# Kernel optimization log

Measured on AMD Instinct MI355X. Metric: run time of the kernel, lower is better.

The kernel has to match this reference:

```python
import jax, jax.numpy as jnp
import numpy as np

S, B, F, U = 8, 65536, 256, 256  # N_species, N_batch, N_feats, N_units (depth=2)


def setup_inputs() -> dict:
    key = jax.random.key(0)
    ks = jax.random.split(key, 9)
    b = jax.random.normal(ks[0], (S, B, F), dtype=jnp.float32)
    # Per-species weights stacked along species axis (equivalent to ModuleList of Linears).
    # nn.Linear default init: U(-1/sqrt(fan_in), 1/sqrt(fan_in)) -- exact dist doesn't matter
    # for a correctness baseline; scale similarly.
    def lin(k, fan_in, shape):
        lim = 1.0 / np.sqrt(fan_in)
        return jax.random.uniform(k, shape, dtype=jnp.float32, minval=-lim, maxval=lim)
    W1 = lin(ks[1], F, (S, F, U)); b1 = lin(ks[2], F, (S, U))
    W2 = lin(ks[3], U, (S, U, U)); b2 = lin(ks[4], U, (S, U))
    W3 = lin(ks[5], U, (S, U, U)); b3 = lin(ks[6], U, (S, U))
    W4 = lin(ks[7], U, (S, U, 1)); b4 = lin(ks[8], U, (S, 1))
    return {"b": b, "W1": W1, "b1": b1, "W2": W2, "b2": b2,
            "W3": W3, "b3": b3, "W4": W4, "b4": b4}


def _leaky(x):
    return jnp.where(x >= 0, x, 0.1 * x)  # LeakyReLU(0.1)


def reference(b, W1, b1, W2, b2, W3, b3, W4, b4):
    # depth == 2 path. Dropout(p=0.01) is identity in eval mode.
    # Per-species batched GEMMs: (S,B,in) x (S,in,out) -> (S,B,out)
    x = _leaky(jnp.einsum('sbf,sfu->sbu', b, W1) + b1[:, None, :])
    x = _leaky(jnp.einsum('sbu,suv->sbv', x, W2) + b2[:, None, :])
    x = _leaky(jnp.einsum('sbu,suv->sbv', x, W3) + b3[:, None, :])
    A = jnp.einsum('sbu,suo->sbo', x, W4) + b4[:, None, :]  # (S, B, 1)
    return jax.nn.sigmoid(A.sum(axis=0))  # (B, 1)
```

## Files before the change

kernel.cpp:

```cpp
#include <hip/hip_runtime.h>

typedef __bf16 bf16x8 __attribute__((ext_vector_type(8)));
typedef float  f32x4  __attribute__((ext_vector_type(4)));
typedef float  fvec4  __attribute__((ext_vector_type(4)));

#define NSPEC 8
#define NB    65536
#define NF    256

__global__ __launch_bounds__(256) void wconv_kernel(
    const float* __restrict__ W1, const float* __restrict__ W2,
    const float* __restrict__ W3, __bf16* __restrict__ WT)
{
    __shared__ float tile[32][33];
    int bid = blockIdx.x;
    int l   = bid >> 9;
    int rem = bid & 511;
    int s   = rem >> 6;
    int tt  = rem & 63;
    int ti  = tt >> 3, tj = tt & 7;
    const float* W   = (l == 0) ? W1 : (l == 1) ? W2 : W3;
    const float* ibs = W + (size_t)s * 65536;
    int c  = threadIdx.x & 31;
    int r0 = threadIdx.x >> 5;
#pragma unroll
    for (int k = 0; k < 4; ++k) {
        int r = r0 + k * 8;
        tile[r][c] = ibs[(ti * 32 + r) * 256 + tj * 32 + c];
    }
    __syncthreads();
    __bf16* obs = WT + ((size_t)(l * 8 + s)) * 65536;
#pragma unroll
    for (int k = 0; k < 4; ++k) {
        int r = r0 + k * 8;
        obs[(tj * 32 + r) * 256 + ti * 32 + c] = (__bf16)tile[c][r];
    }
}

#define GLLD(gp, lp)                                                     \
    __builtin_amdgcn_global_load_lds(                                    \
        (const __attribute__((address_space(1))) char*)(gp),             \
        (__attribute__((address_space(3))) char*)(lp), 16, 0, 0)

#define BAR()                                                            \
    do {                                                                 \
        __builtin_amdgcn_sched_barrier(0);                               \
        asm volatile("s_waitcnt lgkmcnt(0)" ::: "memory");               \
        __builtin_amdgcn_s_barrier();                                    \
        __builtin_amdgcn_sched_barrier(0);                               \
    } while (0)

__global__ __launch_bounds__(256, 2) void mlp_kernel(
    const float* __restrict__ bIn, const float* __restrict__ b1,
    const float* __restrict__ b2,  const float* __restrict__ b3,
    const float* __restrict__ W4,  const float* __restrict__ b4,
    const __bf16* __restrict__ WT, float* __restrict__ P)
{
    __shared__ __align__(16) __bf16 act[64 * 256];
    __shared__ __align__(16) char  wlds[2][16384];

    const int t    = threadIdx.x;
    const int lane = t & 63;
    const int wave = t >> 6;
    const int l15  = lane & 15;
    const int g    = lane >> 4;
    const int wv   = wave * 64;
    const int s    = blockIdx.x >> 10;
    const int row0 = (blockIdx.x & 1023) * 64;
    const int swzB = l15 << 4;
    char* const pA = (char*)act;

    int gll_off[4];
#pragma unroll
    for (int i = 0; i < 4; ++i) {
        int v = wv + i * 16 + (lane >> 2);
        int q = (lane & 3) ^ ((v >> 1) & 3);
        gll_off[i] = v * 512 + q * 16;
    }

    const char* const wt0 = (const char*)(WT + ((size_t)(0 * 8 + s) << 16));
    const char* const wt1 = (const char*)(WT + ((size_t)(1 * 8 + s) << 16));
    const char* const wt2 = (const char*)(WT + ((size_t)(2 * 8 + s) << 16));

#define ISSUE_CHUNK(wtb, gci)                                            \
    do {                                                                 \
        char* lp0 = (char*)&wlds[(gci) & 1][wave * 4096];                \
        GLLD((wtb) + gll_off[0] + ((gci) & 7) * 64, lp0);                \
        GLLD((wtb) + gll_off[1] + ((gci) & 7) * 64, lp0 + 1024);         \
        GLLD((wtb) + gll_off[2] + ((gci) & 7) * 64, lp0 + 2048);         \
        GLLD((wtb) + gll_off[3] + ((gci) & 7) * 64, lp0 + 3072);         \
    } while (0)

    fvec4 bias[3][4];
#pragma unroll
    for (int l = 0; l < 3; ++l) {
        const float* bl = (l == 0 ? b1 : l == 1 ? b2 : b3) + s * 256;
#pragma unroll
        for (int m = 0; m < 4; ++m)
            bias[l][m] = *(const fvec4*)(bl + wv + m * 16 + g * 4);
    }

    const float* src = bIn + ((size_t)s * NB + row0) * NF;
#pragma unroll
    for (int it = 0; it < 16; ++it) {
        int flat = it * 1024 + t * 4;
        int r = flat >> 8;
        int f = flat & 255;
        fvec4 v = __builtin_nontemporal_load((const fvec4*)(src + flat));
        union { __bf16 h[4]; unsigned long long q; } pk;
        pk.h[0] = (__bf16)v[0]; pk.h[1] = (__bf16)v[1];
        pk.h[2] = (__bf16)v[2]; pk.h[3] = (__bf16)v[3];
        *(unsigned long long*)(pA + r * 512 + ((f * 2) ^ ((r & 15) << 4))) = pk.q;
    }

    ISSUE_CHUNK(wt0, 0);
    ISSUE_CHUNK(wt0, 1);
    BAR();

#pragma unroll
    for (int l = 0; l < 3; ++l) {
        f32x4 acc[4][4];
#pragma unroll
        for (int m = 0; m < 4; ++m)
#pragma unroll
            for (int n = 0; n < 4; ++n)
                acc[m][n] = (f32x4){0.f, 0.f, 0.f, 0.f};

#pragma unroll
        for (int ks = 0; ks < 8; ++ks) {
            const int c = l * 8 + ks;
            if (c < 23) asm volatile("s_waitcnt vmcnt(4)" ::: "memory");
            else        asm volatile("s_waitcnt vmcnt(0)" ::: "memory");

            const char* wbuf = (const char*)wlds[ks & 1];
            bf16x8 af[4], bfr[4];
#pragma unroll
            for (int m = 0; m < 4; ++m) {
                int row = wv + m * 16 + l15;
                af[m] = *(const bf16x8*)(wbuf + row * 64 + ((g ^ ((row >> 1) & 3)) << 4));
            }
#pragma unroll
            for (int n = 0; n < 4; ++n)
                bfr[n] = *(const bf16x8*)(pA + (n * 16 + l15) * 512 + ((ks * 64 + g * 16) ^ swzB));

            asm volatile("s_waitcnt lgkmcnt(0)" ::: "memory");
            __builtin_amdgcn_sched_barrier(0);
            const int gci = c + 2;
            if (gci < 24) {
                const char* wtc = (gci < 8) ? wt0 : (gci < 16) ? wt1 : wt2;
                ISSUE_CHUNK(wtc, gci);
            }
            __builtin_amdgcn_sched_barrier(0);

            __builtin_amdgcn_s_setprio(1);
#pragma unroll
            for (int m = 0; m < 4; ++m)
#pragma unroll
                for (int n = 0; n < 4; ++n)
                    acc[m][n] = __builtin_amdgcn_mfma_f32_16x16x32_bf16(af[m], bfr[n], acc[m][n], 0, 0, 0);
            __builtin_amdgcn_s_setprio(0);
        }

        BAR();

#pragma unroll
        for (int m = 0; m < 4; ++m) {
            int vbyte = (wv + m * 16 + g * 4) * 2;
#pragma unroll
            for (int n = 0; n < 4; ++n) {
                union { __bf16 h[4]; unsigned long long q; } pk;
#pragma unroll
                for (int j = 0; j < 4; ++j) {
                    float x = acc[m][n][j] + bias[l][m][j];
                    x = (x >= 0.f) ? x : 0.1f * x;
                    pk.h[j] = (__bf16)x;
                }
                *(unsigned long long*)(pA + (n * 16 + l15) * 512 + (vbyte ^ swzB)) = pk.q;
            }
        }
        BAR();
    }

    const int r4   = t >> 2;
    const int u0   = (t & 3) * 64;
    const int swz4 = (r4 & 15) << 4;
    const float* w4s = W4 + s * 256 + u0;
    float part = 0.f;
#pragma unroll
    for (int i = 0; i < 8; ++i) {
        bf16x8 x = *(const bf16x8*)(pA + r4 * 512 + (((u0 + i * 8) * 2) ^ swz4));
        fvec4 wlo = *(const fvec4*)(w4s + i * 8);
        fvec4 whi = *(const fvec4*)(w4s + i * 8 + 4);
        part += (float)x[0] * wlo[0] + (float)x[1] * wlo[1] +
                (float)x[2] * wlo[2] + (float)x[3] * wlo[3] +
                (float)x[4] * whi[0] + (float)x[5] * whi[1] +
                (float)x[6] * whi[2] + (float)x[7] * whi[3];
    }
    part += __shfl_xor(part, 1);
    part += __shfl_xor(part, 2);
    if ((t & 3) == 0) P[(size_t)s * NB + row0 + r4] = part + b4[s];
}

__global__ __launch_bounds__(256) void reduce_kernel(
    const float* __restrict__ P, float* __restrict__ out)
{
    int i = blockIdx.x * 256 + threadIdx.x;
    float a = 0.f;
#pragma unroll
    for (int sp = 0; sp < NSPEC; ++sp) a += P[(size_t)sp * NB + i];
    out[i] = 1.f / (1.f + __expf(-a));
}

extern "C" void kernel_launch(void* const* d_in, const int* in_sizes, int n_in,
                              void* d_out, int out_size, void* d_ws, size_t ws_size,
                              hipStream_t stream)
{
    const float* bIn = (const float*)d_in[0];
    const float* W1  = (const float*)d_in[1];
    const float* b1  = (const float*)d_in[2];
    const float* W2  = (const float*)d_in[3];
    const float* b2  = (const float*)d_in[4];
    const float* W3  = (const float*)d_in[5];
    const float* b3  = (const float*)d_in[6];
    const float* W4  = (const float*)d_in[7];
    const float* b4  = (const float*)d_in[8];
    __bf16* WT = (__bf16*)d_ws;
    float*  P  = (float*)((char*)d_ws + (3u << 20));

    wconv_kernel<<<1536, 256, 0, stream>>>(W1, W2, W3, WT);
    mlp_kernel<<<8192, 256, 0, stream>>>(bIn, b1, b2, b3, W4, b4, WT, P);
    reduce_kernel<<<NB / 256, 256, 0, stream>>>(P, (float*)d_out);
}
```

Measured before the change: 337.5 us.

## Triple-buffer weight chunks and software-pipeline LDS fragment reads against MFMAs

The weight staging area in LDS grows from two to three 16KB chunk buffers, so global-to-LDS prefetch now runs three chunks ahead instead of two. Operand fragments are loaded into two alternating register sets, so the LDS reads for slice k+1 are issued before the MFMAs for slice k, hiding LDS latency behind the matrix math. The aim is to cut the stalls where the MFMA units wait on global and LDS loads. In exchange, LDS use per block rises to about 80KB and register pressure goes up from the doubled fragment sets, which could hurt occupancy under the two-blocks-per-CU launch bound.

```diff
diff --git a/kernel.cpp b/kernel.cpp
--- a/kernel.cpp
+++ b/kernel.cpp
@@ -57,7 +57,7 @@
     const __bf16* __restrict__ WT, float* __restrict__ P)
 {
     __shared__ __align__(16) __bf16 act[64 * 256];
-    __shared__ __align__(16) char  wlds[2][16384];
+    __shared__ __align__(16) char  wlds[3][16384];
 
     const int t    = threadIdx.x;
     const int lane = t & 63;
@@ -84,11 +84,38 @@
 
 #define ISSUE_CHUNK(wtb, gci)                                            \
     do {                                                                 \
-        char* lp0 = (char*)&wlds[(gci) & 1][wave * 4096];                \
+        char* lp0 = (char*)&wlds[(gci) % 3][wave * 4096];                \
         GLLD((wtb) + gll_off[0] + ((gci) & 7) * 64, lp0);                \
         GLLD((wtb) + gll_off[1] + ((gci) & 7) * 64, lp0 + 1024);         \
         GLLD((wtb) + gll_off[2] + ((gci) & 7) * 64, lp0 + 2048);         \
         GLLD((wtb) + gll_off[3] + ((gci) & 7) * 64, lp0 + 3072);         \
+    } while (0)
+
+#define READ_SET(AF, BF, gci, kslice)                                    \
+    do {                                                                 \
+        const char* wbuf_ = (const char*)wlds[(gci) % 3];                \
+        _Pragma("unroll")                                                \
+        for (int m_ = 0; m_ < 4; ++m_) {                                 \
+            int row_ = wv + m_ * 16 + l15;                               \
+            AF[m_] = *(const bf16x8*)(wbuf_ + row_ * 64 +                \
+                                      ((g ^ ((row_ >> 1) & 3)) << 4));   \
+        }                                                                \
+        _Pragma("unroll")                                                \
+        for (int n_ = 0; n_ < 4; ++n_)                                   \
+            BF[n_] = *(const bf16x8*)(pA + (n_ * 16 + l15) * 512 +       \
+                                      (((kslice) * 64 + g * 16) ^ swzB));\
+    } while (0)
+
+#define MFMA_SET(AF, BF)                                                 \
+    do {                                                                 \
+        __builtin_amdgcn_s_setprio(1);                                   \
+        _Pragma("unroll")                                                \
+        for (int m_ = 0; m_ < 4; ++m_)                                   \
+            _Pragma("unroll")                                            \
+            for (int n_ = 0; n_ < 4; ++n_)                               \
+                acc[m_][n_] = __builtin_amdgcn_mfma_f32_16x16x32_bf16(   \
+                    AF[m_], BF[n_], acc[m_][n_], 0, 0, 0);               \
+        __builtin_amdgcn_s_setprio(0);                                   \
     } while (0)
 
     fvec4 bias[3][4];
@@ -115,10 +142,12 @@
 
     ISSUE_CHUNK(wt0, 0);
     ISSUE_CHUNK(wt0, 1);
+    ISSUE_CHUNK(wt0, 2);
     BAR();
 
 #pragma unroll
     for (int l = 0; l < 3; ++l) {
+        const int c0 = l * 8;
         f32x4 acc[4][4];
 #pragma unroll
         for (int m = 0; m < 4; ++m)
@@ -126,39 +155,27 @@
             for (int n = 0; n < 4; ++n)
                 acc[m][n] = (f32x4){0.f, 0.f, 0.f, 0.f};
 
+        bf16x8 afA[4], bfrA[4], afB[4], bfrB[4];
+        asm volatile("s_waitcnt vmcnt(8)" ::: "memory");
+        READ_SET(afA, bfrA, c0, 0);
+
 #pragma unroll
         for (int ks = 0; ks < 8; ++ks) {
-            const int c = l * 8 + ks;
-            if (c < 23) asm volatile("s_waitcnt vmcnt(4)" ::: "memory");
-            else        asm volatile("s_waitcnt vmcnt(0)" ::: "memory");
-
-            const char* wbuf = (const char*)wlds[ks & 1];
-            bf16x8 af[4], bfr[4];
-#pragma unroll
-            for (int m = 0; m < 4; ++m) {
-                int row = wv + m * 16 + l15;
-                af[m] = *(const bf16x8*)(wbuf + row * 64 + ((g ^ ((row >> 1) & 3)) << 4));
+            const int c = c0 + ks;
+            if (ks < 7) {
+                if (c <= 21) asm volatile("s_waitcnt vmcnt(4)" ::: "memory");
+                else         asm volatile("s_waitcnt vmcnt(0)" ::: "memory");
+                if ((ks & 1) == 0) READ_SET(afB, bfrB, c + 1, ks + 1);
+                else               READ_SET(afA, bfrA, c + 1, ks + 1);
             }
-#pragma unroll
-            for (int n = 0; n < 4; ++n)
-                bfr[n] = *(const bf16x8*)(pA + (n * 16 + l15) * 512 + ((ks * 64 + g * 16) ^ swzB));
-
+            if ((ks & 1) == 0) MFMA_SET(afA, bfrA);
+            else               MFMA_SET(afB, bfrB);
             asm volatile("s_waitcnt lgkmcnt(0)" ::: "memory");
-            __builtin_amdgcn_sched_barrier(0);
-            const int gci = c + 2;
-            if (gci < 24) {
-                const char* wtc = (gci < 8) ? wt0 : (gci < 16) ? wt1 : wt2;
-                ISSUE_CHUNK(wtc, gci);
+            if (c + 3 <= 23) {
+                const char* wtc = (c + 3 < 8) ? wt0 : (c + 3 < 16) ? wt1 : wt2;
+                ISSUE_CHUNK(wtc, c + 3);
             }
             __builtin_amdgcn_sched_barrier(0);
-
-            __builtin_amdgcn_s_setprio(1);
-#pragma unroll
-            for (int m = 0; m < 4; ++m)
-#pragma unroll
-                for (int n = 0; n < 4; ++n)
-                    acc[m][n] = __builtin_amdgcn_mfma_f32_16x16x32_bf16(af[m], bfr[n], acc[m][n], 0, 0, 0);
-            __builtin_amdgcn_s_setprio(0);
         }
 
         BAR();
```

Measured after the change: 352.1 us. 1.04x slower.
